# Kernel optimization log

Measured on AMD Instinct MI355X. Metric: run time of the kernel, lower is better.

The kernel has to match this reference:

```python
import jax, jax.numpy as jnp
import numpy as np

HIDDEN_DIM = 128


def setup_inputs() -> dict:
    key = jax.random.key(0)
    k1, k2, k3, k4, k5 = jax.random.split(key, 5)
    B, M, N2, D = 4, 4096, 8192, 128
    return {
        "x": jax.random.normal(k1, (B, M, D), dtype=jnp.float32),
        "cond": jax.random.normal(k2, (B, N2, D), dtype=jnp.float32),
        "mask": jax.random.normal(k3, (B, M, N2 // 2), dtype=jnp.float32),
        "Wq": jax.random.normal(k4, (HIDDEN_DIM, D), dtype=jnp.float32) / np.sqrt(D),
        "Wkv": jax.random.normal(k5, (HIDDEN_DIM, D), dtype=jnp.float32) / np.sqrt(D),
    }


def reference(x, cond, mask, Wq, Wkv):
    # q: [b, m, d]; kv: [b, 2n, d] chunked along the SEQUENCE dim (dim=-2)
    q = jnp.einsum('bmi,di->bmd', x, Wq)
    kv = jnp.einsum('bni,di->bnd', cond, Wkv)
    k, v = jnp.split(kv, 2, axis=-2)          # each [b, n, d]
    scale = 1.0 / np.sqrt(HIDDEN_DIM).astype(np.float32)
    qk = jnp.einsum('bmd,bnd->bmn', q, k) * scale
    p = jax.nn.softmax(qk, axis=-1) + mask    # post-softmax mask add (as in source)
    return jnp.einsum('bmn,bnd->bmd', p, v)
```

## Files before the change

### kernel.cpp

```cpp
#include <hip/hip_runtime.h>


typedef __attribute__((ext_vector_type(8))) short bf16x8;
typedef __attribute__((ext_vector_type(4))) float f32x4;

static constexpr float kScale = 0.08838834764831845f;
static constexpr float kLog2e = 1.4426950408889634f;

__device__ __forceinline__ unsigned short f2bf(float f) {
  unsigned int u = __float_as_uint(f);
  u = (u + 0x7fffu + ((u >> 16) & 1u)) >> 16;
  return (unsigned short)u;
}

__device__ __forceinline__ float fast_exp2(float v) {
#if __has_builtin(__builtin_amdgcn_exp2f)
  return __builtin_amdgcn_exp2f(v);
#else
  return exp2f(v);
#endif
}

__global__ __launch_bounds__(256) void proj_kernel(
    const float* __restrict__ x, const float* __restrict__ cond,
    const float* __restrict__ Wq, const float* __restrict__ Wkv,
    unsigned short* __restrict__ qws, unsigned short* __restrict__ kws,
    unsigned short* __restrict__ vTws)
{
  __shared__ __align__(16) unsigned short ldsT[128][88];
  const int bid = blockIdx.x;
  const int tid = threadIdx.x;
  const int wave = tid >> 6;
  const int l = tid & 63;
  const int l15 = l & 15, l4 = l >> 4;

  const float* src; const float* W;
  int mode; size_t row0;
  if (bid < 256) { mode = 0; src = x; W = Wq; row0 = (size_t)bid * 64; }
  else {
    row0 = (size_t)(bid - 256) * 64;
    src = cond; W = Wkv;
    mode = ((int)(row0 & 8191) < 4096) ? 1 : 2;
  }
  const size_t rw = row0 + wave * 16;

  bf16x8 af[4];
  {
    const float* rp = src + (rw + l15) * 128 + l4 * 8;
    #pragma unroll
    for (int ks = 0; ks < 4; ks++) {
      float t[8];
      *(float4*)&t[0] = *(const float4*)(rp + ks * 32);
      *(float4*)&t[4] = *(const float4*)(rp + ks * 32 + 4);
      bf16x8 a;
      #pragma unroll
      for (int j = 0; j < 8; j++) a[j] = (short)f2bf(t[j]);
      af[ks] = a;
    }
  }

  f32x4 acc[8];
  #pragma unroll
  for (int d = 0; d < 8; d++) acc[d] = (f32x4){0.f, 0.f, 0.f, 0.f};

  #pragma unroll
  for (int d = 0; d < 8; d++) {
    const float* wp = W + (d * 16 + l15) * 128 + l4 * 8;
    #pragma unroll
    for (int ks = 0; ks < 4; ks++) {
      float t[8];
      *(float4*)&t[0] = *(const float4*)(wp + ks * 32);
      *(float4*)&t[4] = *(const float4*)(wp + ks * 32 + 4);
      bf16x8 wf;
      #pragma unroll
      for (int j = 0; j < 8; j++) wf[j] = (short)f2bf(t[j]);
      acc[d] = __builtin_amdgcn_mfma_f32_16x16x32_bf16(af[ks], wf, acc[d], 0, 0, 0);
    }
  }

  if (mode < 2) {
    size_t obase; unsigned short* outp;
    if (mode == 0) { outp = qws; obase = rw; }
    else { outp = kws; obase = (rw >> 13) * 4096 + (rw & 8191); }
    #pragma unroll
    for (int d = 0; d < 8; d++)
      #pragma unroll
      for (int r = 0; r < 4; r++)
        outp[(obase + l4 * 4 + r) * 128 + d * 16 + l15] = f2bf(acc[d][r]);
  } else {
    #pragma unroll
    for (int d = 0; d < 8; d++)
      #pragma unroll
      for (int r = 0; r < 4; r++)
        ldsT[d * 16 + l15][wave * 16 + l4 * 4 + r] = f2bf(acc[d][r]);
    __syncthreads();
    const size_t b = row0 >> 13;
    const int n0 = (int)(row0 & 8191) - 4096;
    const int dd = tid >> 1, half = tid & 1;
    const unsigned short* sp = &ldsT[dd][half * 32];
    unsigned short* gp = vTws + ((size_t)b * 128 + dd) * 4096 + n0 + half * 32;
    #pragma unroll
    for (int i = 0; i < 4; i++)
      *(int4*)(gp + i * 8) = *(const int4*)(sp + i * 8);
  }
}

__global__ __launch_bounds__(512) void attn_kernel(
    const unsigned short* __restrict__ qws,
    const unsigned short* __restrict__ kws,
    const unsigned short* __restrict__ vTws,
    const float* __restrict__ mask,
    float* __restrict__ out)
{
  __shared__ __align__(16) unsigned short pbuf[2][8][16][72];
  __shared__ float stats[2][64];

  const int bid = blockIdx.x;
  const int xcd = bid & 7, grp = bid >> 3;
  const int b = xcd >> 1;
  const int m0 = (grp * 2 + (xcd & 1)) * 64;

  const int tid = threadIdx.x;
  const int w = tid >> 6, l = tid & 63;
  const int rg = w & 3, nh = w >> 2;
  const int l15 = l & 15, l4 = l >> 4;

  bf16x8 qf[4];
  {
    const unsigned short* qp = qws + ((size_t)b * 4096 + m0 + rg * 16 + l15) * 128 + l4 * 8;
    #pragma unroll
    for (int ks = 0; ks < 4; ks++) qf[ks] = *(const bf16x8*)(qp + ks * 32);
  }

  f32x4 acc1[8], acc2[8];
  #pragma unroll
  for (int d = 0; d < 8; d++) { acc1[d] = (f32x4){0,0,0,0}; acc2[d] = (f32x4){0,0,0,0}; }
  float lsum[4] = {0.f, 0.f, 0.f, 0.f};

  const unsigned short* kbase = kws  + (size_t)b * 4096 * 128;
  const unsigned short* vbase = vTws + (size_t)b * 128 * 4096;
  const float* mbase = mask + ((size_t)b * 4096 + m0 + rg * 16) * 4096;

  for (int nt = 0; nt < 32; nt++) {
    const int n0 = nh * 2048 + nt * 64;

    f32x4 sacc[4];
    #pragma unroll
    for (int ns = 0; ns < 4; ns++) {
      sacc[ns] = (f32x4){0,0,0,0};
      const unsigned short* kp = kbase + (size_t)(n0 + ns * 16 + l15) * 128 + l4 * 8;
      #pragma unroll
      for (int ks = 0; ks < 4; ks++) {
        bf16x8 kf = *(const bf16x8*)(kp + ks * 32);
        sacc[ns] = __builtin_amdgcn_mfma_f32_16x16x32_bf16(qf[ks], kf, sacc[ns], 0, 0, 0);
      }
    }

    #pragma unroll
    for (int ns = 0; ns < 4; ns++) {
      #pragma unroll
      for (int r = 0; r < 4; r++) {
        float e = fast_exp2(sacc[ns][r] * (kScale * kLog2e));
        lsum[r] += e;
        pbuf[0][w][l4 * 4 + r][ns * 16 + l15] = f2bf(e);
      }
    }

    #pragma unroll
    for (int i = 0; i < 4; i++) {
      const int r = i * 4 + l4, c = l15 * 4;
      float4 mv = *(const float4*)(mbase + (size_t)r * 4096 + n0 + c);
      ushort4 mm = make_ushort4(f2bf(mv.x), f2bf(mv.y), f2bf(mv.z), f2bf(mv.w));
      *(ushort4*)&pbuf[1][w][r][c] = mm;
    }

    bf16x8 a1[2], a2[2];
    #pragma unroll
    for (int ks = 0; ks < 2; ks++) {
      a1[ks] = *(const bf16x8*)&pbuf[0][w][l15][ks * 32 + l4 * 8];
      a2[ks] = *(const bf16x8*)&pbuf[1][w][l15][ks * 32 + l4 * 8];
    }
    #pragma unroll
    for (int d = 0; d < 8; d++) {
      const unsigned short* vp = vbase + (size_t)(d * 16 + l15) * 4096 + n0 + l4 * 8;
      #pragma unroll
      for (int ks = 0; ks < 2; ks++) {
        bf16x8 vf = *(const bf16x8*)(vp + ks * 32);
        acc1[d] = __builtin_amdgcn_mfma_f32_16x16x32_bf16(a1[ks], vf, acc1[d], 0, 0, 0);
        acc2[d] = __builtin_amdgcn_mfma_f32_16x16x32_bf16(a2[ks], vf, acc2[d], 0, 0, 0);
      }
    }
  }

  #pragma unroll
  for (int r = 0; r < 4; r++) {
    float s = lsum[r];
    s += __shfl_xor(s, 1); s += __shfl_xor(s, 2);
    s += __shfl_xor(s, 4); s += __shfl_xor(s, 8);
    lsum[r] = s;
  }
  if (l15 == 0) {
    #pragma unroll
    for (int r = 0; r < 4; r++) stats[nh][rg * 16 + l4 * 4 + r] = lsum[r];
  }
  __syncthreads();

  float rl[4];
  #pragma unroll
  for (int r = 0; r < 4; r++) {
    const int row = rg * 16 + l4 * 4 + r;
    rl[r] = 1.0f / (stats[0][row] + stats[1][row]);
  }

  float* cb = (float*)pbuf;
  if (nh == 1) {
    #pragma unroll
    for (int d = 0; d < 8; d++)
      #pragma unroll
      for (int r = 0; r < 4; r++)
        cb[(rg * 16 + l4 * 4 + r) * 128 + d * 16 + l15] = acc1[d][r] * rl[r] + acc2[d][r];
  }
  __syncthreads();
  if (nh == 0) {
    float* op = out + ((size_t)b * 4096 + m0) * 128;
    #pragma unroll
    for (int d = 0; d < 8; d++)
      #pragma unroll
      for (int r = 0; r < 4; r++) {
        const int row = rg * 16 + l4 * 4 + r;
        op[(size_t)row * 128 + d * 16 + l15] =
            acc1[d][r] * rl[r] + acc2[d][r] + cb[row * 128 + d * 16 + l15];
      }
  }
}

extern "C" void kernel_launch(void* const* d_in, const int* in_sizes, int n_in,
                              void* d_out, int out_size, void* d_ws, size_t ws_size,
                              hipStream_t stream) {
  const float* x    = (const float*)d_in[0];
  const float* cond = (const float*)d_in[1];
  const float* mask = (const float*)d_in[2];
  const float* Wq   = (const float*)d_in[3];
  const float* Wkv  = (const float*)d_in[4];

  unsigned short* qws = (unsigned short*)d_ws;
  unsigned short* kws = qws + (size_t)4 * 4096 * 128;
  unsigned short* vT  = kws + (size_t)4 * 4096 * 128;

  hipLaunchKernelGGL(proj_kernel, dim3(768), dim3(256), 0, stream,
                     x, cond, Wq, Wkv, qws, kws, vT);
  hipLaunchKernelGGL(attn_kernel, dim3(256), dim3(512), 0, stream,
                     qws, kws, vT, mask, (float*)d_out);
}
```

Before: 621.8 us.

## Prefetch K and mask tiles in registers, pre-convert weights, coalesce projection stores

Result: faster. 593.3 us (-4.6%).

```diff
diff --git a/kernel.cpp b/kernel.cpp
--- a/kernel.cpp
+++ b/kernel.cpp
@@ -1,11 +1,11 @@
 #include <hip/hip_runtime.h>
+#include <hip/hip_bf16.h>
 
 
 typedef __attribute__((ext_vector_type(8))) short bf16x8;
 typedef __attribute__((ext_vector_type(4))) float f32x4;
 
-static constexpr float kScale = 0.08838834764831845f;
-static constexpr float kLog2e = 1.4426950408889634f;
+static constexpr float kSc = 0.08838834764831845f * 1.4426950408889634f;
 
 __device__ __forceinline__ unsigned short f2bf(float f) {
   unsigned int u = __float_as_uint(f);
@@ -21,83 +21,99 @@
 #endif
 }
 
+__global__ __launch_bounds__(256) void wcvt_kernel(
+    const float* __restrict__ Wq, const float* __restrict__ Wkv,
+    unsigned short* __restrict__ wqb, unsigned short* __restrict__ wkb)
+{
+  const int t = blockIdx.x * 256 + threadIdx.x;
+  #pragma unroll
+  for (int s = 0; s < 2; s++) {
+    const float* src = s ? Wkv : Wq;
+    unsigned short* dst = s ? wkb : wqb;
+    float4 a = ((const float4*)src)[t * 2], b = ((const float4*)src)[t * 2 + 1];
+    ushort4 o0 = make_ushort4(f2bf(a.x), f2bf(a.y), f2bf(a.z), f2bf(a.w));
+    ushort4 o1 = make_ushort4(f2bf(b.x), f2bf(b.y), f2bf(b.z), f2bf(b.w));
+    ((ushort4*)dst)[t * 2] = o0;
+    ((ushort4*)dst)[t * 2 + 1] = o1;
+  }
+}
+
 __global__ __launch_bounds__(256) void proj_kernel(
     const float* __restrict__ x, const float* __restrict__ cond,
-    const float* __restrict__ Wq, const float* __restrict__ Wkv,
+    const unsigned short* __restrict__ wqb, const unsigned short* __restrict__ wkb,
     unsigned short* __restrict__ qws, unsigned short* __restrict__ kws,
     unsigned short* __restrict__ vTws)
 {
-  __shared__ __align__(16) unsigned short ldsT[128][88];
-  const int bid = blockIdx.x;
-  const int tid = threadIdx.x;
-  const int wave = tid >> 6;
-  const int l = tid & 63;
-  const int l15 = l & 15, l4 = l >> 4;
-
-  const float* src; const float* W;
+  __shared__ __align__(16) unsigned short lds[128 * 88];
+  const int bid = blockIdx.x, tid = threadIdx.x;
+  const int wave = tid >> 6, l = tid & 63, l15 = l & 15, l4 = l >> 4;
+
+  const float* src; const unsigned short* W;
   int mode; size_t row0;
-  if (bid < 256) { mode = 0; src = x; W = Wq; row0 = (size_t)bid * 64; }
-  else {
-    row0 = (size_t)(bid - 256) * 64;
-    src = cond; W = Wkv;
-    mode = ((int)(row0 & 8191) < 4096) ? 1 : 2;
-  }
+  if (bid < 256) { mode = 0; src = x; W = wqb; row0 = (size_t)bid * 64; }
+  else { row0 = (size_t)(bid - 256) * 64; src = cond; W = wkb;
+         mode = ((int)(row0 & 8191) < 4096) ? 1 : 2; }
   const size_t rw = row0 + wave * 16;
 
+  f32x4 ar[8];
+  const float* rp = src + (rw + l15) * 128 + l4 * 8;
+  #pragma unroll
+  for (int ks = 0; ks < 4; ks++) {
+    ar[2 * ks]     = *(const f32x4*)(rp + ks * 32);
+    ar[2 * ks + 1] = *(const f32x4*)(rp + ks * 32 + 4);
+  }
   bf16x8 af[4];
-  {
-    const float* rp = src + (rw + l15) * 128 + l4 * 8;
+  #pragma unroll
+  for (int ks = 0; ks < 4; ks++) {
+    bf16x8 a;
+    #pragma unroll
+    for (int j = 0; j < 4; j++) {
+      a[j]     = (short)f2bf(ar[2 * ks][j]);
+      a[4 + j] = (short)f2bf(ar[2 * ks + 1][j]);
+    }
+    af[ks] = a;
+  }
+
+  f32x4 acc[8];
+  #pragma unroll
+  for (int d = 0; d < 8; d++) acc[d] = (f32x4){0.f, 0.f, 0.f, 0.f};
+
+  const unsigned short* wp = W + l15 * 128 + l4 * 8;
+  #pragma unroll
+  for (int d = 0; d < 8; d++)
     #pragma unroll
     for (int ks = 0; ks < 4; ks++) {
-      float t[8];
-      *(float4*)&t[0] = *(const float4*)(rp + ks * 32);
-      *(float4*)&t[4] = *(const float4*)(rp + ks * 32 + 4);
-      bf16x8 a;
-      #pragma unroll
-      for (int j = 0; j < 8; j++) a[j] = (short)f2bf(t[j]);
-      af[ks] = a;
-    }
-  }
-
-  f32x4 acc[8];
-  #pragma unroll
-  for (int d = 0; d < 8; d++) acc[d] = (f32x4){0.f, 0.f, 0.f, 0.f};
-
-  #pragma unroll
-  for (int d = 0; d < 8; d++) {
-    const float* wp = W + (d * 16 + l15) * 128 + l4 * 8;
-    #pragma unroll
-    for (int ks = 0; ks < 4; ks++) {
-      float t[8];
-      *(float4*)&t[0] = *(const float4*)(wp + ks * 32);
-      *(float4*)&t[4] = *(const float4*)(wp + ks * 32 + 4);
-      bf16x8 wf;
-      #pragma unroll
-      for (int j = 0; j < 8; j++) wf[j] = (short)f2bf(t[j]);
+      bf16x8 wf = *(const bf16x8*)(wp + d * 16 * 128 + ks * 32);
       acc[d] = __builtin_amdgcn_mfma_f32_16x16x32_bf16(af[ks], wf, acc[d], 0, 0, 0);
     }
-  }
 
   if (mode < 2) {
+    #pragma unroll
+    for (int d = 0; d < 8; d++)
+      #pragma unroll
+      for (int r = 0; r < 4; r++)
+        lds[(wave * 16 + l4 * 4 + r) * 136 + d * 16 + l15] = f2bf(acc[d][r]);
+    __syncthreads();
     size_t obase; unsigned short* outp;
-    if (mode == 0) { outp = qws; obase = rw; }
-    else { outp = kws; obase = (rw >> 13) * 4096 + (rw & 8191); }
+    if (mode == 0) { outp = qws; obase = row0; }
+    else { outp = kws; obase = (row0 >> 13) * 4096 + (row0 & 8191); }
+    const int row = tid >> 2, ch = (tid & 3) * 32;
+    const unsigned short* sp = lds + row * 136 + ch;
+    unsigned short* gp = outp + (obase + row) * 128 + ch;
+    #pragma unroll
+    for (int i = 0; i < 4; i++)
+      *(int4*)(gp + i * 8) = *(const int4*)(sp + i * 8);
+  } else {
     #pragma unroll
     for (int d = 0; d < 8; d++)
       #pragma unroll
       for (int r = 0; r < 4; r++)
-        outp[(obase + l4 * 4 + r) * 128 + d * 16 + l15] = f2bf(acc[d][r]);
-  } else {
-    #pragma unroll
-    for (int d = 0; d < 8; d++)
-      #pragma unroll
-      for (int r = 0; r < 4; r++)
-        ldsT[d * 16 + l15][wave * 16 + l4 * 4 + r] = f2bf(acc[d][r]);
+        lds[(d * 16 + l15) * 88 + wave * 16 + l4 * 4 + r] = f2bf(acc[d][r]);
     __syncthreads();
     const size_t b = row0 >> 13;
     const int n0 = (int)(row0 & 8191) - 4096;
     const int dd = tid >> 1, half = tid & 1;
-    const unsigned short* sp = &ldsT[dd][half * 32];
+    const unsigned short* sp = lds + dd * 88 + half * 32;
     unsigned short* gp = vTws + ((size_t)b * 128 + dd) * 4096 + n0 + half * 32;
     #pragma unroll
     for (int i = 0; i < 4; i++)
@@ -105,14 +121,15 @@
   }
 }
 
-__global__ __launch_bounds__(512) void attn_kernel(
+__global__ __launch_bounds__(512, 2) void attn_kernel(
     const unsigned short* __restrict__ qws,
     const unsigned short* __restrict__ kws,
     const unsigned short* __restrict__ vTws,
     const float* __restrict__ mask,
     float* __restrict__ out)
 {
-  __shared__ __align__(16) unsigned short pbuf[2][8][16][72];
+  __shared__ __align__(16) unsigned short pbuf[8][16][72];
+  __shared__ __align__(16) float cb[64][128];
   __shared__ float stats[2][64];
 
   const int bid = blockIdx.x;
@@ -120,8 +137,7 @@
   const int b = xcd >> 1;
   const int m0 = (grp * 2 + (xcd & 1)) * 64;
 
-  const int tid = threadIdx.x;
-  const int w = tid >> 6, l = tid & 63;
+  const int tid = threadIdx.x, w = tid >> 6, l = tid & 63;
   const int rg = w & 3, nh = w >> 2;
   const int l15 = l & 15, l4 = l >> 4;
 
@@ -137,59 +153,99 @@
   for (int d = 0; d < 8; d++) { acc1[d] = (f32x4){0,0,0,0}; acc2[d] = (f32x4){0,0,0,0}; }
   float lsum[4] = {0.f, 0.f, 0.f, 0.f};
 
-  const unsigned short* kbase = kws  + (size_t)b * 4096 * 128;
-  const unsigned short* vbase = vTws + (size_t)b * 128 * 4096;
-  const float* mbase = mask + ((size_t)b * 4096 + m0 + rg * 16) * 4096;
+  const unsigned short* kbase = kws  + (size_t)b * 4096 * 128 + (size_t)l15 * 128 + l4 * 8;
+  const unsigned short* vbase = vTws + (size_t)b * 128 * 4096 + (size_t)l15 * 4096 + l4 * 8;
+  const float* mbase = mask + ((size_t)b * 4096 + m0 + rg * 16 + l15) * 4096 + l4 * 8;
+
+  const int nbase = nh * 2048;
+
+  bf16x8 kf[4][4];
+  #pragma unroll
+  for (int ns = 0; ns < 4; ns++)
+    #pragma unroll
+    for (int ks = 0; ks < 4; ks++)
+      kf[ns][ks] = *(const bf16x8*)(kbase + (size_t)(nbase + ns * 16) * 128 + ks * 32);
+  f32x4 mreg[4];
+  #pragma unroll
+  for (int ks = 0; ks < 2; ks++)
+    #pragma unroll
+    for (int h = 0; h < 2; h++)
+      mreg[ks * 2 + h] = *(const f32x4*)(mbase + nbase + ks * 32 + h * 4);
 
   for (int nt = 0; nt < 32; nt++) {
-    const int n0 = nh * 2048 + nt * 64;
+    const int n0 = nbase + nt * 64;
+    const int nn = nbase + (nt < 31 ? nt + 1 : 31) * 64;
+
+    bf16x8 vf[16];
+    #pragma unroll
+    for (int d = 0; d < 4; d++)
+      #pragma unroll
+      for (int ks = 0; ks < 2; ks++)
+        vf[d * 2 + ks] = *(const bf16x8*)(vbase + (size_t)(d * 16) * 4096 + n0 + ks * 32);
 
     f32x4 sacc[4];
     #pragma unroll
     for (int ns = 0; ns < 4; ns++) {
       sacc[ns] = (f32x4){0,0,0,0};
-      const unsigned short* kp = kbase + (size_t)(n0 + ns * 16 + l15) * 128 + l4 * 8;
-      #pragma unroll
-      for (int ks = 0; ks < 4; ks++) {
-        bf16x8 kf = *(const bf16x8*)(kp + ks * 32);
-        sacc[ns] = __builtin_amdgcn_mfma_f32_16x16x32_bf16(qf[ks], kf, sacc[ns], 0, 0, 0);
+      #pragma unroll
+      for (int ks = 0; ks < 4; ks++)
+        sacc[ns] = __builtin_amdgcn_mfma_f32_16x16x32_bf16(qf[ks], kf[ns][ks], sacc[ns], 0, 0, 0);
+    }
+    #pragma unroll
+    for (int ns = 0; ns < 4; ns++)
+      #pragma unroll
+      for (int ks = 0; ks < 4; ks++)
+        kf[ns][ks] = *(const bf16x8*)(kbase + (size_t)(nn + ns * 16) * 128 + ks * 32);
+
+    bf16x8 a2[2];
+    #pragma unroll
+    for (int ks = 0; ks < 2; ks++) {
+      bf16x8 t;
+      #pragma unroll
+      for (int j = 0; j < 4; j++) {
+        t[j]     = (short)f2bf(mreg[ks * 2][j]);
+        t[4 + j] = (short)f2bf(mreg[ks * 2 + 1][j]);
       }
+      a2[ks] = t;
     }
-
-    #pragma unroll
-    for (int ns = 0; ns < 4; ns++) {
+    #pragma unroll
+    for (int ks = 0; ks < 2; ks++)
+      #pragma unroll
+      for (int h = 0; h < 2; h++)
+        mreg[ks * 2 + h] = *(const f32x4*)(mbase + nn + ks * 32 + h * 4);
+
+    #pragma unroll
+    for (int ns = 0; ns < 4; ns++)
       #pragma unroll
       for (int r = 0; r < 4; r++) {
-        float e = fast_exp2(sacc[ns][r] * (kScale * kLog2e));
+        float e = fast_exp2(sacc[ns][r] * kSc);
         lsum[r] += e;
-        pbuf[0][w][l4 * 4 + r][ns * 16 + l15] = f2bf(e);
+        pbuf[w][l4 * 4 + r][ns * 16 + l15] = f2bf(e);
       }
-    }
-
-    #pragma unroll
-    for (int i = 0; i < 4; i++) {
-      const int r = i * 4 + l4, c = l15 * 4;
-      float4 mv = *(const float4*)(mbase + (size_t)r * 4096 + n0 + c);
-      ushort4 mm = make_ushort4(f2bf(mv.x), f2bf(mv.y), f2bf(mv.z), f2bf(mv.w));
-      *(ushort4*)&pbuf[1][w][r][c] = mm;
-    }
-
-    bf16x8 a1[2], a2[2];
-    #pragma unroll
-    for (int ks = 0; ks < 2; ks++) {
-      a1[ks] = *(const bf16x8*)&pbuf[0][w][l15][ks * 32 + l4 * 8];
-      a2[ks] = *(const bf16x8*)&pbuf[1][w][l15][ks * 32 + l4 * 8];
-    }
-    #pragma unroll
-    for (int d = 0; d < 8; d++) {
-      const unsigned short* vp = vbase + (size_t)(d * 16 + l15) * 4096 + n0 + l4 * 8;
-      #pragma unroll
-      for (int ks = 0; ks < 2; ks++) {
-        bf16x8 vf = *(const bf16x8*)(vp + ks * 32);
-        acc1[d] = __builtin_amdgcn_mfma_f32_16x16x32_bf16(a1[ks], vf, acc1[d], 0, 0, 0);
-        acc2[d] = __builtin_amdgcn_mfma_f32_16x16x32_bf16(a2[ks], vf, acc2[d], 0, 0, 0);
-      }
-    }
+
+    #pragma unroll
+    for (int d = 4; d < 8; d++)
+      #pragma unroll
+      for (int ks = 0; ks < 2; ks++)
+        vf[d * 2 + ks] = *(const bf16x8*)(vbase + (size_t)(d * 16) * 4096 + n0 + ks * 32);
+
+    bf16x8 a1[2];
+    #pragma unroll
+    for (int ks = 0; ks < 2; ks++)
+      a1[ks] = *(const bf16x8*)&pbuf[w][l15][ks * 32 + l4 * 8];
+
+    __builtin_amdgcn_s_setprio(1);
+    #pragma unroll
+    for (int d = 0; d < 8; d++)
+      #pragma unroll
+      for (int ks = 0; ks < 2; ks++)
+        acc2[d] = __builtin_amdgcn_mfma_f32_16x16x32_bf16(a2[ks], vf[d * 2 + ks], acc2[d], 0, 0, 0);
+    #pragma unroll
+    for (int d = 0; d < 8; d++)
+      #pragma unroll
+      for (int ks = 0; ks < 2; ks++)
+        acc1[d] = __builtin_amdgcn_mfma_f32_16x16x32_bf16(a1[ks], vf[d * 2 + ks], acc1[d], 0, 0, 0);
+    __builtin_amdgcn_s_setprio(0);
   }
 
   #pragma unroll
@@ -199,27 +255,22 @@
     s += __shfl_xor(s, 4); s += __shfl_xor(s, 8);
     lsum[r] = s;
   }
-  if (l15 == 0) {
+  if (l15 == 0)
     #pragma unroll
     for (int r = 0; r < 4; r++) stats[nh][rg * 16 + l4 * 4 + r] = lsum[r];
-  }
   __syncthreads();
 
   float rl[4];
   #pragma unroll
-  for (int r = 0; r < 4; r++) {
-    const int row = rg * 16 + l4 * 4 + r;
-    rl[r] = 1.0f / (stats[0][row] + stats[1][row]);
-  }
-
-  float* cb = (float*)pbuf;
-  if (nh == 1) {
+  for (int r = 0; r < 4; r++)
+    rl[r] = 1.0f / (stats[0][rg * 16 + l4 * 4 + r] + stats[1][rg * 16 + l4 * 4 + r]);
+
+  if (nh == 1)
     #pragma unroll
     for (int d = 0; d < 8; d++)
       #pragma unroll
       for (int r = 0; r < 4; r++)
-        cb[(rg * 16 + l4 * 4 + r) * 128 + d * 16 + l15] = acc1[d][r] * rl[r] + acc2[d][r];
-  }
+        cb[rg * 16 + l4 * 4 + r][d * 16 + l15] = acc1[d][r] * rl[r] + acc2[d][r];
   __syncthreads();
   if (nh == 0) {
     float* op = out + ((size_t)b * 4096 + m0) * 128;
@@ -229,7 +280,7 @@
       for (int r = 0; r < 4; r++) {
         const int row = rg * 16 + l4 * 4 + r;
         op[(size_t)row * 128 + d * 16 + l15] =
-            acc1[d][r] * rl[r] + acc2[d][r] + cb[row * 128 + d * 16 + l15];
+            acc1[d][r] * rl[r] + acc2[d][r] + cb[row][d * 16 + l15];
       }
   }
 }
@@ -246,9 +297,12 @@
   unsigned short* qws = (unsigned short*)d_ws;
   unsigned short* kws = qws + (size_t)4 * 4096 * 128;
   unsigned short* vT  = kws + (size_t)4 * 4096 * 128;
-
+  unsigned short* wqb = vT  + (size_t)4 * 128 * 4096;
+  unsigned short* wkb = wqb + 128 * 128;
+
+  hipLaunchKernelGGL(wcvt_kernel, dim3(8), dim3(256), 0, stream, Wq, Wkv, wqb, wkb);
   hipLaunchKernelGGL(proj_kernel, dim3(768), dim3(256), 0, stream,
-                     x, cond, Wq, Wkv, qws, kws, vT);
+                     x, cond, wqb, wkb, qws, kws, vT);
   hipLaunchKernelGGL(attn_kernel, dim3(256), dim3(512), 0, stream,
                      qws, kws, vT, mask, (float*)d_out);
 }
```
